# Optimization experiments

Measured on AMD Instinct MI355X. Metric: run time of the kernel, lower is better.

## Reference

```python
import jax, jax.numpy as jnp
import numpy as np

# ---- static config (matches init_kwargs) ----
CANVAS = (18, 24, 24)
TILE = (6, 8, 8)
KERNEL = (1, 3, 3)
TEXT_LEN = 320
B, H, D = 1, 4, 128
SCALE = 1.0 / np.sqrt(D)

TT, TH, TW = TILE
NT, NH, NW = CANVAS[0] // TT, CANVAS[1] // TH, CANVAS[2] // TW
BLOCK = TT * TH * TW                      # 384
N_IMG = NT * NH * NW                      # 27 image blocks
IMG_LEN = CANVAS[0] * CANVAS[1] * CANVAS[2]
TEXT_BLOCKS = -(-TEXT_LEN // BLOCK)       # 1
TEXT_PAD = TEXT_BLOCKS * BLOCK - TEXT_LEN # 64
TOTAL_BLOCKS = N_IMG + TEXT_BLOCKS        # 28
SEQ_LEN = IMG_LEN + TEXT_LEN


def _sta_kv_blocks():
    """Per-image-block allowed KV block indices (incl. text blocks), [N_IMG, n_allowed]."""
    kt, kh, kw = KERNEL
    idx = np.arange(N_IMG)
    qt = idx // (NH * NW)
    qh = (idx % (NH * NW)) // NW
    qw = idx % NW
    ct = np.clip(qt, kt // 2, NT - 1 - kt // 2)
    ch = np.clip(qh, kh // 2, NH - 1 - kh // 2)
    cw = np.clip(qw, kw // 2, NW - 1 - kw // 2)
    mask = ((np.abs(ct[:, None] - qt[None, :]) <= kt // 2)
            & (np.abs(ch[:, None] - qh[None, :]) <= kh // 2)
            & (np.abs(cw[:, None] - qw[None, :]) <= kw // 2))
    text_ids = np.arange(N_IMG, TOTAL_BLOCKS)
    rows = [np.concatenate([np.nonzero(mask[i])[0], text_ids]) for i in range(N_IMG)]
    return np.stack(rows)  # uniform n_allowed by clamping

KV_BLOCKS = jnp.asarray(_sta_kv_blocks())  # [N_IMG, NA]
NA = KV_BLOCKS.shape[1]                    # 10


def _tile(x):
    # [B,H,IMG_LEN,D] raster -> tile order
    x = x.reshape(B, H, NT, TT, NH, TH, NW, TW, D)
    x = x.transpose(0, 1, 2, 4, 6, 3, 5, 7, 8)
    return x.reshape(B, H, N_IMG * BLOCK, D)


def _untile(x):
    x = x.reshape(B, H, NT, NH, NW, TT, TH, TW, D)
    x = x.transpose(0, 1, 2, 5, 3, 6, 4, 7, 8)
    return x.reshape(B, H, IMG_LEN, D)


def _prep(x):
    # split image/text, tile image, zero-pad text to block multiple, concat
    img = _tile(x[:, :, :IMG_LEN])
    txt = jnp.pad(x[:, :, IMG_LEN:], ((0, 0), (0, 0), (0, TEXT_PAD), (0, 0)))
    return jnp.concatenate([img, txt], axis=2)  # [B,H,TOTAL_BLOCKS*BLOCK,D]


def setup_inputs() -> dict:
    key = jax.random.key(0)
    kq, kk, kv = jax.random.split(key, 3)
    shape = (B, H, SEQ_LEN, D)
    return {
        "q": jax.random.normal(kq, shape, dtype=jnp.float32),
        "k": jax.random.normal(kk, shape, dtype=jnp.float32),
        "v": jax.random.normal(kv, shape, dtype=jnp.float32),
    }


def reference(q, k, v):
    Q, K, V = _prep(q), _prep(k), _prep(v)
    Qb = Q.reshape(B, H, TOTAL_BLOCKS, BLOCK, D)
    Kb = K.reshape(B, H, TOTAL_BLOCKS, BLOCK, D)
    Vb = V.reshape(B, H, TOTAL_BLOCKS, BLOCK, D)

    # ---- image blocks: grouped block-sparse attention (KV gathered per block) ----
    Qi = Qb[:, :, :N_IMG]                                   # [B,H,N_IMG,BLOCK,D]
    Ki = Kb[:, :, KV_BLOCKS].reshape(B, H, N_IMG, NA * BLOCK, D)
    Vi = Vb[:, :, KV_BLOCKS].reshape(B, H, N_IMG, NA * BLOCK, D)
    s = jnp.einsum("bhnqd,bhnkd->bhnqk", Qi, Ki) * SCALE
    p = jax.nn.softmax(s, axis=-1)
    oi = jnp.einsum("bhnqk,bhnkd->bhnqd", p, Vi)            # [B,H,N_IMG,BLOCK,D]

    # ---- text blocks: dense attention over full (tiled img + padded text) KV ----
    Qt = Qb[:, :, N_IMG:].reshape(B, H, TEXT_BLOCKS * BLOCK, D)
    st = jnp.einsum("bhqd,bhkd->bhqk", Qt, K) * SCALE
    ot = jnp.einsum("bhqk,bhkd->bhqd", jax.nn.softmax(st, axis=-1), V)

    img_out = _untile(oi.reshape(B, H, N_IMG * BLOCK, D))
    return jnp.concatenate([img_out, ot[:, :, :TEXT_LEN]], axis=2)  # [B,H,SEQ_LEN,D]
```

## Files before the change

### kernel.cpp

```cpp
#include <hip/hip_runtime.h>

#define SEQ      10688
#define IMG_LEN  10368
#define TEXT_LEN 320
#define DH       128
#define NHEADS   4
#define SLAB     3456
#define KVC      32
#define QT       128
#define NIT      81
#define NTT      3
#define NCH_TXT  334
#define NCH_IMG  118
#define SCALEL2E 0.12751744518924593f
#define FIXM     16.0f
#define PADTERM  0.0009765625f

typedef __bf16 bf16x8 __attribute__((ext_vector_type(8)));
typedef __bf16 bf16x4 __attribute__((ext_vector_type(4)));
typedef float  f32x4  __attribute__((ext_vector_type(4)));

__device__ __forceinline__ unsigned pk2bf(float a, float b) {
    union { __bf16 h[2]; unsigned u; } t;
    t.h[0] = (__bf16)a; t.h[1] = (__bf16)b;
    return t.u;
}

__device__ __forceinline__ float fexp2(float x) {
    float r;
    asm("v_exp_f32 %0, %1" : "=v"(r) : "v"(x));
    return r;
}
__device__ __forceinline__ unsigned cvtpk(float a, float b) {
    unsigned r;
    asm("v_cvt_pk_bf16_f32 %0, %1, %2" : "=v"(r) : "v"(a), "v"(b));
    return r;
}

__device__ __forceinline__ bf16x8 as_bf16x8(uint4 u) {
    union { uint4 a; bf16x8 v; } t; t.a = u; return t.v;
}

__device__ __forceinline__ void split_range(int total, int nsplit, int s, int& c0, int& n) {
    const int q = total / nsplit, r = total % nsplit;
    if (s < r) { c0 = s * (q + 1); n = q + 1; }
    else       { c0 = r * (q + 1) + (s - r) * q; n = q; }
}

template<int TS, int IS> struct Geo {
    static constexpr int NTXTB = NHEADS * NTT * TS;
    static constexpr int NIMGB = NHEADS * NIT * IS;
    static constexpr int NPID  = NTXTB + NIMGB;
    static constexpr size_t WS_FLOATS = (size_t)NPID * (QT * DH + QT * 2);
};
#define KB_BYTES ((size_t)NHEADS * SEQ * DH * 2)

__global__ __launch_bounds__(256) void sta_prep(const float* __restrict__ Kg,
                                                const float* __restrict__ Vg,
                                                uint4* __restrict__ Kf,
                                                uint4* __restrict__ Vf) {
    __shared__ float T[64][65];
    const int b = blockIdx.x;
    if (b < NHEADS * 334) {
        const int hb = b / 334, chunk = b % 334;
        const float* src = Kg + ((size_t)hb * SEQ + chunk * 32) * DH;
        const int t = threadIdx.x;
        #pragma unroll
        for (int i = 0; i < 2; ++i) {
            const int oidx = t + 256 * i;
            const int frag = oidx >> 6, lane = oidx & 63;
            const int c = frag >> 1, kt = frag & 1;
            const int row = kt * 16 + (lane & 15);
            const int col = c * 32 + (lane >> 4) * 8;
            float4 a = *(const float4*)(src + (size_t)row * DH + col);
            float4 d = *(const float4*)(src + (size_t)row * DH + col + 4);
            uint4 u; u.x = pk2bf(a.x, a.y); u.y = pk2bf(a.z, a.w);
                     u.z = pk2bf(d.x, d.y); u.w = pk2bf(d.z, d.w);
            Kf[((size_t)(hb * 334 + chunk) * 8 + frag) * 64 + lane] = u;
        }
    } else {
        const int bb = b - NHEADS * 334;
        const int dhalf = bb & 1, kvt = (bb >> 1) % 167, h = (bb >> 1) / 167;
        const float* src = Vg + ((size_t)h * SEQ + kvt * 64) * DH + dhalf * 64;
        const int t = threadIdx.x;
        const int col = t & 63, r4 = t >> 6;
        #pragma unroll
        for (int i = 0; i < 16; ++i) {
            const int row = i * 4 + r4;
            T[row][col] = src[(size_t)row * DH + col];
        }
        __syncthreads();
        const int lane = t & 63, q = t & 15, gg = lane >> 4;
        #pragma unroll
        for (int i = 0; i < 2; ++i) {
            const int idx = (t >> 6) * 2 + i;
            const int ch2 = idx >> 2, kt = (idx >> 1) & 1, dtp = idx & 1;
            const int kvl = ch2 * 32 + kt * 16 + gg * 4;
            const int dle = dtp * 32 + q;
            const int dlo = dle + 16;
            uint4 u;
            u.x = pk2bf(T[kvl][dle],     T[kvl + 1][dle]);
            u.y = pk2bf(T[kvl + 2][dle], T[kvl + 3][dle]);
            u.z = pk2bf(T[kvl][dlo],     T[kvl + 1][dlo]);
            u.w = pk2bf(T[kvl + 2][dlo], T[kvl + 3][dlo]);
            const size_t o4 = ((size_t)(h * 334 + kvt * 2 + ch2) * 8
                               + kt * 4 + dhalf * 2 + dtp) * 64 + lane;
            Vf[o4] = u;
        }
    }
}

template<int TS, int IS, bool SPLIT>
__global__ __launch_bounds__(256) void sta_attn(const float* __restrict__ Qg,
                                                const uint4* __restrict__ Kf,
                                                const uint4* __restrict__ Vf,
                                                float* __restrict__ Og,
                                                float* __restrict__ Opart,
                                                float* __restrict__ Ml) {
    using G = Geo<TS, IS>;
    const int tid  = threadIdx.x;
    const int lane = tid & 63;
    const int wv   = tid >> 6;
    const int q    = lane & 15;
    const int g    = lane >> 4;

    int b = blockIdx.x;
    int head, qbase, nch, ch0, kvb0, pid = 0;
    bool isText;
    if (b < G::NTXTB) {
        int tb = b / TS, s = b % TS;
        head = tb / NTT; qbase = IMG_LEN + (tb % NTT) * QT;
        isText = true; kvb0 = 0;
        split_range(NCH_TXT, TS, s, ch0, nch);
        pid = b;
    } else {
        int bb = b - G::NTXTB; int tile = bb / IS, s = bb % IS;
        head = tile / NIT; qbase = (tile % NIT) * QT;
        isText = false; kvb0 = (qbase / SLAB) * SLAB;
        split_range(NCH_IMG, IS, s, ch0, nch);
        pid = G::NTXTB + bb;
    }

    const size_t hoff = (size_t)head * SEQ * DH;
    const float* Qh = Qg + hoff;
    const uint4* kfh = Kf + (size_t)head * 334 * 512 + lane;
    const uint4* vfh = Vf + (size_t)head * 334 * 512 + lane;

    bf16x8 qf[2][4];
    #pragma unroll
    for (int n = 0; n < 2; ++n) {
        int qr = qbase + wv * 32 + n * 16 + q;
        if (qr > SEQ - 1) qr = SEQ - 1;
        const float* qp = Qh + (size_t)qr * DH;
        #pragma unroll
        for (int c = 0; c < 4; ++c) {
            float4 a = *(const float4*)(qp + c * 32 + g * 8);
            float4 d = *(const float4*)(qp + c * 32 + g * 8 + 4);
            union { unsigned u[4]; bf16x8 v; } t;
            t.u[0] = pk2bf(a.x * SCALEL2E, a.y * SCALEL2E);
            t.u[1] = pk2bf(a.z * SCALEL2E, a.w * SCALEL2E);
            t.u[2] = pk2bf(d.x * SCALEL2E, d.y * SCALEL2E);
            t.u[3] = pk2bf(d.z * SCALEL2E, d.w * SCALEL2E);
            qf[n][c] = t.v;
        }
    }

    f32x4 o[2][8];
    #pragma unroll
    for (int n = 0; n < 2; ++n)
        #pragma unroll
        for (int dt = 0; dt < 8; ++dt) o[n][dt] = f32x4{0.f, 0.f, 0.f, 0.f};
    float lsum[2] = {0.f, 0.f};

    auto kvaddr = [&](int gch) -> int {
        return isText ? gch * KVC
                      : (gch < 108 ? kvb0 + gch * KVC : IMG_LEN + (gch - 108) * KVC);
    };

    uint4 kf4[8];
    {
        const uint4* kp = kfh + (size_t)(kvaddr(ch0) >> 5) * 512;
        #pragma unroll
        for (int f = 0; f < 8; ++f) kf4[f] = kp[f * 64];
    }

    for (int ch = 0; ch < nch; ++ch) {
        const int kb = kvaddr(ch0 + ch);

        const uint4* vp = vfh + (size_t)(kb >> 5) * 512;
        uint4 vf4[8];
        #pragma unroll
        for (int f = 0; f < 8; ++f) vf4[f] = vp[f * 64];

        f32x4 st[2][2];
        #pragma unroll
        for (int n = 0; n < 2; ++n)
            #pragma unroll
            for (int kt = 0; kt < 2; ++kt)
                st[n][kt] = f32x4{-FIXM, -FIXM, -FIXM, -FIXM};
        __builtin_amdgcn_s_setprio(1);
        #pragma unroll
        for (int c = 0; c < 4; ++c) {
            #pragma unroll
            for (int kt = 0; kt < 2; ++kt) {
                bf16x8 kf = as_bf16x8(kf4[c * 2 + kt]);
                st[0][kt] = __builtin_amdgcn_mfma_f32_16x16x32_bf16(kf, qf[0][c], st[0][kt], 0, 0, 0);
                st[1][kt] = __builtin_amdgcn_mfma_f32_16x16x32_bf16(kf, qf[1][c], st[1][kt], 0, 0, 0);
            }
        }
        __builtin_amdgcn_s_setprio(0);

        bf16x4 pkv[2][2];
        #pragma unroll
        for (int n = 0; n < 2; ++n) {
            float ps = 0.f;
            #pragma unroll
            for (int kt = 0; kt < 2; ++kt) {
                float p0 = fexp2(st[n][kt][0]);
                float p1 = fexp2(st[n][kt][1]);
                float p2 = fexp2(st[n][kt][2]);
                float p3 = fexp2(st[n][kt][3]);
                ps += (p0 + p1) + (p2 + p3);
                union { unsigned u[2]; bf16x4 v; } t;
                t.u[0] = cvtpk(p0, p1);
                t.u[1] = cvtpk(p2, p3);
                pkv[n][kt] = t.v;
            }
            lsum[n] += ps;
        }

        if (ch + 1 < nch) {
            const uint4* kp = kfh + (size_t)(kvaddr(ch0 + ch + 1) >> 5) * 512;
            #pragma unroll
            for (int f = 0; f < 8; ++f) kf4[f] = kp[f * 64];
        }

        __builtin_amdgcn_s_setprio(1);
        #pragma unroll
        for (int kt = 0; kt < 2; ++kt) {
            #pragma unroll
            for (int dt = 0; dt < 8; ++dt) {
                bf16x4 vb = ((const bf16x4*)&vf4[kt * 4 + (dt >> 1)])[dt & 1];
                asm("v_mfma_f32_16x16x16_bf16 %0, %1, %2, %0"
                    : "+v"(o[0][dt]) : "v"(pkv[0][kt]), "v"(vb));
                asm("v_mfma_f32_16x16x16_bf16 %0, %1, %2, %0"
                    : "+v"(o[1][dt]) : "v"(pkv[1][kt]), "v"(vb));
            }
        }
        __builtin_amdgcn_s_setprio(0);
    }

    asm volatile("s_nop 7\n\ts_nop 7");

    #pragma unroll
    for (int n = 0; n < 2; ++n) {
        lsum[n] += __shfl_xor(lsum[n], 16);
        lsum[n] += __shfl_xor(lsum[n], 32);
    }

    if constexpr (SPLIT) {
        float* opb = Opart + (size_t)pid * (QT * DH);
        #pragma unroll
        for (int n = 0; n < 2; ++n) {
            #pragma unroll
            for (int r = 0; r < 4; ++r) {
                const int row = wv * 32 + n * 16 + g * 4 + r;
                float* op = opb + row * DH + q;
                #pragma unroll
                for (int dt = 0; dt < 8; ++dt) op[dt * 16] = o[n][dt][r];
            }
            if (g == 0) {
                const int srow = wv * 32 + n * 16 + q;
                Ml[(size_t)pid * (QT * 2) + srow * 2]     = FIXM;
                Ml[(size_t)pid * (QT * 2) + srow * 2 + 1] = lsum[n];
            }
        }
    } else {
        #pragma unroll
        for (int n = 0; n < 2; ++n) {
            const float inv = 1.f / (lsum[n] + PADTERM);
            f32x4 invv;
            #pragma unroll
            for (int r = 0; r < 4; ++r)
                invv[r] = __shfl(inv, (lane & 48) + g * 4 + r);
            #pragma unroll
            for (int r = 0; r < 4; ++r) {
                const int qrow = qbase + wv * 32 + n * 16 + g * 4 + r;
                if (qrow >= SEQ) continue;
                float* op = Og + hoff + (size_t)qrow * DH + q;
                #pragma unroll
                for (int dt = 0; dt < 8; ++dt) op[dt * 16] = o[n][dt][r] * invv[r];
            }
        }
    }
}

template<int S>
__device__ __forceinline__ void merge_body(const float* __restrict__ Opart,
                                           const float* __restrict__ Ml,
                                           float* __restrict__ Og,
                                           int head, int qbase, int pbase,
                                           int row, int c4) {
    if (qbase + row >= SEQ) return;
    float w[S], lv[S];
    float m = -INFINITY;
    #pragma unroll
    for (int s = 0; s < S; ++s) {
        w[s]  = Ml[(size_t)(pbase + s) * (QT * 2) + row * 2];
        lv[s] = Ml[(size_t)(pbase + s) * (QT * 2) + row * 2 + 1];
        m = fmaxf(m, w[s]);
    }
    float L = 64.f * exp2f(-m);
    #pragma unroll
    for (int s = 0; s < S; ++s) { w[s] = exp2f(w[s] - m); L += w[s] * lv[s]; }
    const float inv = 1.f / L;

    float* op = Og + (size_t)head * SEQ * DH + (size_t)(qbase + row) * DH;
    #pragma unroll
    for (int half = 0; half < 2; ++half) {
        const int j = c4 + half * 16;
        float4 acc = make_float4(0.f, 0.f, 0.f, 0.f);
        #pragma unroll
        for (int s = 0; s < S; ++s) {
            const float4 p = *(const float4*)(Opart + (size_t)(pbase + s) * (QT * DH)
                                              + row * DH + j * 4);
            acc.x += w[s] * p.x; acc.y += w[s] * p.y;
            acc.z += w[s] * p.z; acc.w += w[s] * p.w;
        }
        float4 v; v.x = acc.x * inv; v.y = acc.y * inv; v.z = acc.z * inv; v.w = acc.w * inv;
        *(float4*)(op + j * 4) = v;
    }
}

template<int TS, int IS>
__global__ __launch_bounds__(256) void sta_merge(const float* __restrict__ Opart,
                                                 const float* __restrict__ Ml,
                                                 float* __restrict__ Og) {
    const int bb = blockIdx.x;
    const int b = bb >> 3, slice = bb & 7;
    const int t = threadIdx.x;
    const int row = slice * 16 + (t >> 4);
    const int c4  = t & 15;
    if (b < NHEADS * NTT) {
        merge_body<TS>(Opart, Ml, Og, b / NTT, IMG_LEN + (b % NTT) * QT,
                       b * TS, row, c4);
    } else {
        const int tile = b - NHEADS * NTT;
        merge_body<IS>(Opart, Ml, Og, tile / NIT, (tile % NIT) * QT,
                       NHEADS * NTT * TS + tile * IS, row, c4);
    }
}

extern "C" void kernel_launch(void* const* d_in, const int* in_sizes, int n_in,
                              void* d_out, int out_size, void* d_ws, size_t ws_size,
                              hipStream_t stream) {
    const float* Qg = (const float*)d_in[0];
    const float* Kg = (const float*)d_in[1];
    const float* Vg = (const float*)d_in[2];
    float* Og = (float*)d_out;
    char* wsb = (char*)d_ws;

    uint4* Kfb = (uint4*)wsb;
    uint4* Vfb = (uint4*)(wsb + KB_BYTES);
    float* Opart = (float*)(wsb + 2 * KB_BYTES);
    const int nprep  = NHEADS * 334 + NHEADS * 2 * 167;
    const int nmerge = NHEADS * (NTT + NIT) * 8;

    if (ws_size >= 2 * KB_BYTES + Geo<8, 4>::WS_FLOATS * sizeof(float)) {
        float* Ml = Opart + (size_t)Geo<8, 4>::NPID * QT * DH;
        hipLaunchKernelGGL(sta_prep, dim3(nprep), dim3(256), 0, stream, Kg, Vg, Kfb, Vfb);
        hipLaunchKernelGGL((sta_attn<8, 4, true>), dim3(Geo<8, 4>::NPID), dim3(256), 0, stream,
                           Qg, Kfb, Vfb, Og, Opart, Ml);
        hipLaunchKernelGGL((sta_merge<8, 4>), dim3(nmerge), dim3(256), 0, stream,
                           Opart, Ml, Og);
    } else if (ws_size >= 2 * KB_BYTES + Geo<4, 2>::WS_FLOATS * sizeof(float)) {
        float* Ml = Opart + (size_t)Geo<4, 2>::NPID * QT * DH;
        hipLaunchKernelGGL(sta_prep, dim3(nprep), dim3(256), 0, stream, Kg, Vg, Kfb, Vfb);
        hipLaunchKernelGGL((sta_attn<4, 2, true>), dim3(Geo<4, 2>::NPID), dim3(256), 0, stream,
                           Qg, Kfb, Vfb, Og, Opart, Ml);
        hipLaunchKernelGGL((sta_merge<4, 2>), dim3(nmerge), dim3(256), 0, stream,
                           Opart, Ml, Og);
    } else {
        hipLaunchKernelGGL(sta_prep, dim3(nprep), dim3(256), 0, stream, Kg, Vg, Kfb, Vfb);
        hipLaunchKernelGGL((sta_attn<1, 1, false>), dim3(Geo<1, 1>::NPID), dim3(256), 0, stream,
                           Qg, Kfb, Vfb, Og, (float*)nullptr, (float*)nullptr);
    }
}
```

Measured before the change: 144.8 us.

## Use 16x16x32 bf16 MFMA for PV product with repacked V fragments

Rearranges the V preprocessing layout so that each lane's fragment holds 8 kv rows for one d column, which lets the PV accumulation use the wider K=32 MFMA. This halves the number of MFMA issues and removes the hand-written inline asm and the trailing s_nop padding. It also adds a launch_bounds occupancy hint of 2 blocks per CU. The layout change has to match the register layout of the P fragments exactly, otherwise results are wrong.

```diff
diff --git a/kernel.cpp b/kernel.cpp
--- a/kernel.cpp
+++ b/kernel.cpp
@@ -17,7 +17,6 @@
 #define PADTERM  0.0009765625f
 
 typedef __bf16 bf16x8 __attribute__((ext_vector_type(8)));
-typedef __bf16 bf16x4 __attribute__((ext_vector_type(4)));
 typedef float  f32x4  __attribute__((ext_vector_type(4)));
 
 __device__ __forceinline__ unsigned pk2bf(float a, float b) {
@@ -90,33 +89,33 @@
             T[row][col] = src[(size_t)row * DH + col];
         }
         __syncthreads();
-        const int lane = t & 63, q = t & 15, gg = lane >> 4;
+        const int lane = t & 63, dq = t & 15, gg = lane >> 4;
         #pragma unroll
         for (int i = 0; i < 2; ++i) {
             const int idx = (t >> 6) * 2 + i;
-            const int ch2 = idx >> 2, kt = (idx >> 1) & 1, dtp = idx & 1;
-            const int kvl = ch2 * 32 + kt * 16 + gg * 4;
-            const int dle = dtp * 32 + q;
-            const int dlo = dle + 16;
+            const int ch2 = idx >> 2, dtl = idx & 3;
+            const int kvb = ch2 * 32 + gg * 4;
+            const int d = dtl * 16 + dq;
             uint4 u;
-            u.x = pk2bf(T[kvl][dle],     T[kvl + 1][dle]);
-            u.y = pk2bf(T[kvl + 2][dle], T[kvl + 3][dle]);
-            u.z = pk2bf(T[kvl][dlo],     T[kvl + 1][dlo]);
-            u.w = pk2bf(T[kvl + 2][dlo], T[kvl + 3][dlo]);
+            u.x = pk2bf(T[kvb + 0][d],  T[kvb + 1][d]);
+            u.y = pk2bf(T[kvb + 2][d],  T[kvb + 3][d]);
+            u.z = pk2bf(T[kvb + 16][d], T[kvb + 17][d]);
+            u.w = pk2bf(T[kvb + 18][d], T[kvb + 19][d]);
+            const int dtglob = dhalf * 4 + dtl;
             const size_t o4 = ((size_t)(h * 334 + kvt * 2 + ch2) * 8
-                               + kt * 4 + dhalf * 2 + dtp) * 64 + lane;
+                               + dtglob) * 64 + lane;
             Vf[o4] = u;
         }
     }
 }
 
 template<int TS, int IS, bool SPLIT>
-__global__ __launch_bounds__(256) void sta_attn(const float* __restrict__ Qg,
-                                                const uint4* __restrict__ Kf,
-                                                const uint4* __restrict__ Vf,
-                                                float* __restrict__ Og,
-                                                float* __restrict__ Opart,
-                                                float* __restrict__ Ml) {
+__global__ __launch_bounds__(256, 2) void sta_attn(const float* __restrict__ Qg,
+                                                   const uint4* __restrict__ Kf,
+                                                   const uint4* __restrict__ Vf,
+                                                   float* __restrict__ Og,
+                                                   float* __restrict__ Opart,
+                                                   float* __restrict__ Ml) {
     using G = Geo<TS, IS>;
     const int tid  = threadIdx.x;
     const int lane = tid & 63;
@@ -210,10 +209,11 @@
         }
         __builtin_amdgcn_s_setprio(0);
 
-        bf16x4 pkv[2][2];
+        bf16x8 pa[2];
         #pragma unroll
         for (int n = 0; n < 2; ++n) {
             float ps = 0.f;
+            union { unsigned u[4]; bf16x8 v; } t;
             #pragma unroll
             for (int kt = 0; kt < 2; ++kt) {
                 float p0 = fexp2(st[n][kt][0]);
@@ -221,11 +221,10 @@
                 float p2 = fexp2(st[n][kt][2]);
                 float p3 = fexp2(st[n][kt][3]);
                 ps += (p0 + p1) + (p2 + p3);
-                union { unsigned u[2]; bf16x4 v; } t;
-                t.u[0] = cvtpk(p0, p1);
-                t.u[1] = cvtpk(p2, p3);
-                pkv[n][kt] = t.v;
-            }
+                t.u[kt * 2]     = cvtpk(p0, p1);
+                t.u[kt * 2 + 1] = cvtpk(p2, p3);
+            }
+            pa[n] = t.v;
             lsum[n] += ps;
         }
 
@@ -237,20 +236,13 @@
 
         __builtin_amdgcn_s_setprio(1);
         #pragma unroll
-        for (int kt = 0; kt < 2; ++kt) {
-            #pragma unroll
-            for (int dt = 0; dt < 8; ++dt) {
-                bf16x4 vb = ((const bf16x4*)&vf4[kt * 4 + (dt >> 1)])[dt & 1];
-                asm("v_mfma_f32_16x16x16_bf16 %0, %1, %2, %0"
-                    : "+v"(o[0][dt]) : "v"(pkv[0][kt]), "v"(vb));
-                asm("v_mfma_f32_16x16x16_bf16 %0, %1, %2, %0"
-                    : "+v"(o[1][dt]) : "v"(pkv[1][kt]), "v"(vb));
-            }
+        for (int dt = 0; dt < 8; ++dt) {
+            bf16x8 vb = as_bf16x8(vf4[dt]);
+            o[0][dt] = __builtin_amdgcn_mfma_f32_16x16x32_bf16(pa[0], vb, o[0][dt], 0, 0, 0);
+            o[1][dt] = __builtin_amdgcn_mfma_f32_16x16x32_bf16(pa[1], vb, o[1][dt], 0, 0, 0);
         }
         __builtin_amdgcn_s_setprio(0);
     }
-
-    asm volatile("s_nop 7\n\ts_nop 7");
 
     #pragma unroll
     for (int n = 0; n < 2; ++n) {
```

New measurement: 138.3 us. 1.05x faster.
